# Kernel optimization log

Hardware: AMD Instinct MI355X
Metric: run time of the kernel (lower is better)

## Reference

```python
import jax, jax.numpy as jnp
import numpy as np

N = 150000          # active 4D voxels
K = 81              # 3^4 kernel offsets for 4D sparse conv, kernel_size=3
C_HID = 8           # MinkUNet14 INIT_DIM / stem+head planes
B, T, Z, Y, X = 2, 4, 32, 256, 256  # batch + output_grid [T,Z,Y,X]


def setup_inputs() -> dict:
    key = jax.random.key(0)
    k1, k2, k3, k4, k5, k6, k7, k8, k9 = jax.random.split(key, 9)
    feats = jnp.ones((N, 1), dtype=jnp.float32)  # module uses all-ones features
    # precomputed rulebook: neighbor index per kernel offset, with validity mask
    nbr_idx = jax.random.randint(k1, (N, K), 0, N, dtype=jnp.int32)
    nbr_mask = jax.random.randint(k2, (N, K), 0, 2, dtype=jnp.int32)
    # output voxel coordinates (x, y, z, t) and batch index, in-range
    cx = jax.random.randint(k3, (N,), 0, X, dtype=jnp.int32)
    cy = jax.random.randint(k4, (N,), 0, Y, dtype=jnp.int32)
    cz = jax.random.randint(k5, (N,), 0, Z, dtype=jnp.int32)
    ct = jax.random.randint(k6, (N,), 0, T, dtype=jnp.int32)
    coords = jnp.stack([cx, cy, cz, ct], axis=1)
    batch_idx = jax.random.randint(k7, (N,), 0, B, dtype=jnp.int32)
    # conv weights: [K, C_in, C_out]
    w1 = jax.random.normal(k8, (K, 1, C_HID), dtype=jnp.float32) * 0.1
    w2 = jax.random.normal(k9, (K, C_HID, C_HID), dtype=jnp.float32) * 0.05
    w_out = jax.random.normal(jax.random.fold_in(key, 99), (C_HID, 1), dtype=jnp.float32) * 0.1
    return {"feats": feats, "w1": w1, "w2": w2, "w_out": w_out,
            "nbr_idx": nbr_idx, "nbr_mask": nbr_mask,
            "coords": coords, "batch_idx": batch_idx}


def reference(feats, w1, w2, w_out, nbr_idx, nbr_mask, coords, batch_idx):
    mask = nbr_mask.astype(feats.dtype)[:, :, None]  # [N, K, 1]

    def sparse_conv(x, w):
        # gather-GEMM-scatter sparse conv: gather neighbors, implicit GEMM over offsets
        g = x[nbr_idx] * mask                 # [N, K, C_in]
        return jnp.einsum('nkc,kcd->nd', g, w)  # [N, C_out]

    h = jax.nn.relu(sparse_conv(feats, w1))   # 1 -> 8
    h = jax.nn.relu(sparse_conv(h, w2))       # 8 -> 8
    out_feats = h @ w_out                     # 8 -> 1 (out_channels=1)

    # dense scatter: dense_F[b, :, x, y, z, t] = feats, then permute(0,5,4,3,2,1)+squeeze
    # equivalent to scattering directly into [B, T, Z, Y, X]
    dense = jnp.zeros((B, T, Z, Y, X), dtype=feats.dtype)
    dense = dense.at[batch_idx, coords[:, 3], coords[:, 2], coords[:, 1], coords[:, 0]].set(out_feats[:, 0])
    return dense
```

## Files before the change

kernel.cpp:

```cpp
#include <hip/hip_runtime.h>
#include <hip/hip_fp16.h>


#define KK 81
#define CH 8
#define NS 21
#define TT 4
#define ZZ 32
#define YY 256
#define XX 256

typedef __attribute__((ext_vector_type(8))) _Float16 half8;
typedef __attribute__((ext_vector_type(4))) float f32x4;

__global__ __launch_bounds__(256) void k_h1b(const float* __restrict__ w1,
                                             const float* __restrict__ w2,
                                             const int* __restrict__ nbr_mask,
                                             half8* __restrict__ h1,
                                             uint4* __restrict__ bits4,
                                             half8* __restrict__ Btab, int n_total) {
    __shared__ int lm[256 * 27];
    const int tid = threadIdx.x;
    const int n0 = blockIdx.x * 256;
    const int n = n0 + tid;

    if (blockIdx.x < NS && tid < 64) {
        int s = blockIdx.x, q = tid >> 4, d = tid & 15;
        int kk = 4 * s + q;
        half8 b;
#pragma unroll
        for (int j = 0; j < CH; j++)
            b[j] = (d < CH && kk < KK) ? (_Float16)w2[(kk * CH + j) * CH + d]
                                       : (_Float16)0.f;
        Btab[s * 64 + tid] = b;
    }
    if (blockIdx.x == 0 && tid == 0) {
        half8 z;
#pragma unroll
        for (int c = 0; c < CH; c++) z[c] = (_Float16)0.f;
        h1[n_total] = z;
    }

    float acc[CH] = {0.f, 0.f, 0.f, 0.f, 0.f, 0.f, 0.f, 0.f};
    unsigned cb[3];
#pragma unroll
    for (int ch = 0; ch < 3; ch++) {
#pragma unroll
        for (int j = 0; j < 27; j++) {
            int i = tid + j * 256;
            int r = i / 27, c = i - r * 27;
            int srcn = n0 + r; if (srcn >= n_total) srcn = n_total - 1;
            lm[i] = nbr_mask[(long)srcn * KK + ch * 27 + c];
        }
        __syncthreads();
        unsigned cbits = 0;
        const int* row = lm + tid * 27;
#pragma unroll
        for (int kk = 0; kk < 27; kk++) {
            int m = row[kk];
            cbits |= (unsigned)(m & 1) << kk;
            float fm = (float)m;
            const float* wp = w1 + (ch * 27 + kk) * CH;
#pragma unroll
            for (int c = 0; c < CH; c++) acc[c] += fm * wp[c];
        }
        cb[ch] = cbits;
        __syncthreads();
    }

    if (n < n_total) {
        half8 r;
#pragma unroll
        for (int c = 0; c < CH; c++) r[c] = (_Float16)fmaxf(acc[c], 0.f);
        h1[n] = r;
        uint4 bw;
        bw.x = cb[0] | (cb[1] << 27);
        bw.y = (cb[1] >> 5) | (cb[2] << 22);
        bw.z = cb[2] >> 10;
        bw.w = 0u;
        bits4[n] = bw;
    }
}

__global__ __launch_bounds__(256, 4) void k_h2m(const half8* __restrict__ h1,
                                                const half8* __restrict__ Btab,
                                                const int* __restrict__ nbr_idx,
                                                const uint4* __restrict__ bits4,
                                                const float* __restrict__ w_out,
                                                float* __restrict__ outf,
                                                int n_total) {
    __shared__ int4 sB[NS * 64];
    __shared__ int  sidx[4 * 1300];
    const int tid = threadIdx.x;
    const int lane = tid & 63, wid = tid >> 6;
    const int m = lane & 15, q = lane >> 4;

    const int rw = blockIdx.x * 64 + (wid << 4);
    int wb = rw;
    if (wb + 16 > n_total) wb = n_total - 16;

    {
        int4* dst = (int4*)(sidx + wid * 1300);
        const int4* gsrc = (const int4*)(nbr_idx + (size_t)wb * KK);
#pragma unroll
        for (int j = 0; j < 6; j++) {
            int li = lane + j * 64;
            if (li < 324) dst[li] = gsrc[li];
        }
    }
    {
        const int4* gB = (const int4*)Btab;
#pragma unroll
        for (int j = 0; j < 6; j++) {
            int i = tid + j * 256;
            if (i < NS * 64) sB[i] = gB[i];
        }
    }
    __syncthreads();

    const int rowc = wb + m;
    const uint4 bw = bits4[rowc];
    const int* mi = sidx + wid * 1300 + m * KK + q;

    f32x4 acc0 = {0.f, 0.f, 0.f, 0.f};
    f32x4 acc1 = {0.f, 0.f, 0.f, 0.f};
#pragma unroll
    for (int s = 0; s < NS; s++) {
        const unsigned word = (s < 8) ? bw.x : (s < 16) ? bw.y : bw.z;
        const unsigned bit = (word >> ((4 * s + q) & 31)) & 1u;
        const unsigned ixr = (unsigned)mi[4 * s];
        const unsigned ix = bit ? ixr : (unsigned)n_total;
        half8 a = h1[ix];
        half8 b = *(const half8*)&sB[s * 64 + lane];
        if (s & 1) acc1 = __builtin_amdgcn_mfma_f32_16x16x32_f16(a, b, acc1, 0, 0, 0);
        else       acc0 = __builtin_amdgcn_mfma_f32_16x16x32_f16(a, b, acc0, 0, 0, 0);
    }
    f32x4 acc = acc0 + acc1;

    float wo = (m < CH) ? w_out[m] : 0.f;
    float v0 = fmaxf(acc[0], 0.f) * wo, v1 = fmaxf(acc[1], 0.f) * wo;
    float v2 = fmaxf(acc[2], 0.f) * wo, v3 = fmaxf(acc[3], 0.f) * wo;
#pragma unroll
    for (int off = 1; off < 16; off <<= 1) {
        v0 += __shfl_xor(v0, off, 16);
        v1 += __shfl_xor(v1, off, 16);
        v2 += __shfl_xor(v2, off, 16);
        v3 += __shfl_xor(v3, off, 16);
    }
    if (m == 0) {
        int gn = rw + q * 4;
        if (gn + 0 < n_total) outf[gn + 0] = v0;
        if (gn + 1 < n_total) outf[gn + 1] = v1;
        if (gn + 2 < n_total) outf[gn + 2] = v2;
        if (gn + 3 < n_total) outf[gn + 3] = v3;
    }
}

__device__ __forceinline__ int cell_of(const int* coords, const int* batch, int n) {
    int4 c = *(const int4*)(coords + 4 * n);
    int b = batch[n];
    return (((b * TT + c.w) * ZZ + c.z) * YY + c.y) * XX + c.x;
}

__global__ __launch_bounds__(256) void k_scat_max(const int* __restrict__ coords,
                                                  const int* __restrict__ batch,
                                                  int* __restrict__ dsti, int n_total) {
    int n = blockIdx.x * blockDim.x + threadIdx.x;
    if (n >= n_total) return;
    atomicMax(dsti + cell_of(coords, batch, n), n + 1);
}

__global__ __launch_bounds__(256) void k_scat_write(const int* __restrict__ coords,
                                                    const int* __restrict__ batch,
                                                    const float* __restrict__ outf,
                                                    int* dsti, float* dstf, int n_total) {
    int n = blockIdx.x * blockDim.x + threadIdx.x;
    if (n >= n_total) return;
    int cell = cell_of(coords, batch, n);
    if (dsti[cell] == n + 1) dstf[cell] = outf[n];
}

extern "C" void kernel_launch(void* const* d_in, const int* in_sizes, int n_in,
                              void* d_out, int out_size, void* d_ws, size_t ws_size,
                              hipStream_t stream) {
    const float* w1       = (const float*)d_in[1];
    const float* w2       = (const float*)d_in[2];
    const float* w_out    = (const float*)d_in[3];
    const int*   nbr_idx  = (const int*)d_in[4];
    const int*   nbr_mask = (const int*)d_in[5];
    const int*   coords   = (const int*)d_in[6];
    const int*   batch    = (const int*)d_in[7];

    int n_total = in_sizes[0];

    half8* h1    = (half8*)d_ws;
    uint4* bits4 = (uint4*)((char*)d_ws + (size_t)(n_total + 1) * sizeof(half8));
    float* outf  = (float*)((char*)bits4 + (size_t)n_total * sizeof(uint4));
    half8* Btab  = (half8*)(outf + n_total);
    float* out   = (float*)d_out;

    hipMemsetAsync(out, 0, (size_t)out_size * sizeof(float), stream);

    int nb = (n_total + 255) / 256;
    k_h1b<<<nb, 256, 0, stream>>>(w1, w2, nbr_mask, h1, bits4, Btab, n_total);
    int nb2 = (n_total + 63) / 64;
    k_h2m<<<nb2, 256, 0, stream>>>(h1, Btab, nbr_idx, bits4, w_out, outf, n_total);
    k_scat_max<<<nb, 256, 0, stream>>>(coords, batch, (int*)out, n_total);
    k_scat_write<<<nb, 256, 0, stream>>>(coords, batch, outf, (int*)out, out, n_total);
}
```

Baseline: 210.0 us.

## Fuse scatter atomicMax and final write into conv kernels, skip masked gathers

Moves the last-writer atomicMax pass into the first conv kernel and the conditional dense write into the MFMA kernel's epilogue. This removes two kernel launches and the intermediate outf buffer round trip. It also replaces the redirect-to-zero-row gather with a predicated load, so masked neighbors issue no memory access. The trade-off is that atomics now compete with h1 work, and the epilogue adds scalar loads of coords and the winner index on a single lane per row group.

```diff
diff --git a/kernel.cpp b/kernel.cpp
--- a/kernel.cpp
+++ b/kernel.cpp
@@ -13,16 +13,27 @@
 typedef __attribute__((ext_vector_type(8))) _Float16 half8;
 typedef __attribute__((ext_vector_type(4))) float f32x4;
 
+__device__ __forceinline__ int cell_of(const int* coords, const int* batch, int n) {
+    int4 c = *(const int4*)(coords + 4 * n);
+    int b = batch[n];
+    return (((b * TT + c.w) * ZZ + c.z) * YY + c.y) * XX + c.x;
+}
+
 __global__ __launch_bounds__(256) void k_h1b(const float* __restrict__ w1,
                                              const float* __restrict__ w2,
                                              const int* __restrict__ nbr_mask,
+                                             const int* __restrict__ coords,
+                                             const int* __restrict__ batch,
                                              half8* __restrict__ h1,
                                              uint4* __restrict__ bits4,
-                                             half8* __restrict__ Btab, int n_total) {
+                                             half8* __restrict__ Btab,
+                                             int* __restrict__ dsti, int n_total) {
     __shared__ int lm[256 * 27];
     const int tid = threadIdx.x;
     const int n0 = blockIdx.x * 256;
     const int n = n0 + tid;
+
+    if (n < n_total) atomicMax(dsti + cell_of(coords, batch, n), n + 1);
 
     if (blockIdx.x < NS && tid < 64) {
         int s = blockIdx.x, q = tid >> 4, d = tid & 15;
@@ -87,7 +98,9 @@
                                                 const int* __restrict__ nbr_idx,
                                                 const uint4* __restrict__ bits4,
                                                 const float* __restrict__ w_out,
-                                                float* __restrict__ outf,
+                                                const int* __restrict__ coords,
+                                                const int* __restrict__ batch,
+                                                float* __restrict__ dstf,
                                                 int n_total) {
     __shared__ int4 sB[NS * 64];
     __shared__ int  sidx[4 * 1300];
@@ -129,8 +142,9 @@
         const unsigned word = (s < 8) ? bw.x : (s < 16) ? bw.y : bw.z;
         const unsigned bit = (word >> ((4 * s + q) & 31)) & 1u;
         const unsigned ixr = (unsigned)mi[4 * s];
-        const unsigned ix = bit ? ixr : (unsigned)n_total;
-        half8 a = h1[ix];
+        half8 a = {(_Float16)0.f, (_Float16)0.f, (_Float16)0.f, (_Float16)0.f,
+                   (_Float16)0.f, (_Float16)0.f, (_Float16)0.f, (_Float16)0.f};
+        if (bit) a = h1[ixr];
         half8 b = *(const half8*)&sB[s * 64 + lane];
         if (s & 1) acc1 = __builtin_amdgcn_mfma_f32_16x16x32_f16(a, b, acc1, 0, 0, 0);
         else       acc0 = __builtin_amdgcn_mfma_f32_16x16x32_f16(a, b, acc0, 0, 0, 0);
@@ -148,36 +162,17 @@
         v3 += __shfl_xor(v3, off, 16);
     }
     if (m == 0) {
+        const int* dsti = (const int*)dstf;
         int gn = rw + q * 4;
-        if (gn + 0 < n_total) outf[gn + 0] = v0;
-        if (gn + 1 < n_total) outf[gn + 1] = v1;
-        if (gn + 2 < n_total) outf[gn + 2] = v2;
-        if (gn + 3 < n_total) outf[gn + 3] = v3;
-    }
-}
-
-__device__ __forceinline__ int cell_of(const int* coords, const int* batch, int n) {
-    int4 c = *(const int4*)(coords + 4 * n);
-    int b = batch[n];
-    return (((b * TT + c.w) * ZZ + c.z) * YY + c.y) * XX + c.x;
-}
-
-__global__ __launch_bounds__(256) void k_scat_max(const int* __restrict__ coords,
-                                                  const int* __restrict__ batch,
-                                                  int* __restrict__ dsti, int n_total) {
-    int n = blockIdx.x * blockDim.x + threadIdx.x;
-    if (n >= n_total) return;
-    atomicMax(dsti + cell_of(coords, batch, n), n + 1);
-}
-
-__global__ __launch_bounds__(256) void k_scat_write(const int* __restrict__ coords,
-                                                    const int* __restrict__ batch,
-                                                    const float* __restrict__ outf,
-                                                    int* dsti, float* dstf, int n_total) {
-    int n = blockIdx.x * blockDim.x + threadIdx.x;
-    if (n >= n_total) return;
-    int cell = cell_of(coords, batch, n);
-    if (dsti[cell] == n + 1) dstf[cell] = outf[n];
+        if (gn + 0 < n_total) { int c0 = cell_of(coords, batch, gn + 0);
+                                if (dsti[c0] == gn + 1) dstf[c0] = v0; }
+        if (gn + 1 < n_total) { int c1 = cell_of(coords, batch, gn + 1);
+                                if (dsti[c1] == gn + 2) dstf[c1] = v1; }
+        if (gn + 2 < n_total) { int c2 = cell_of(coords, batch, gn + 2);
+                                if (dsti[c2] == gn + 3) dstf[c2] = v2; }
+        if (gn + 3 < n_total) { int c3 = cell_of(coords, batch, gn + 3);
+                                if (dsti[c3] == gn + 4) dstf[c3] = v3; }
+    }
 }
 
 extern "C" void kernel_launch(void* const* d_in, const int* in_sizes, int n_in,
@@ -195,16 +190,15 @@
 
     half8* h1    = (half8*)d_ws;
     uint4* bits4 = (uint4*)((char*)d_ws + (size_t)(n_total + 1) * sizeof(half8));
-    float* outf  = (float*)((char*)bits4 + (size_t)n_total * sizeof(uint4));
-    half8* Btab  = (half8*)(outf + n_total);
+    half8* Btab  = (half8*)((char*)bits4 + (size_t)n_total * sizeof(uint4));
     float* out   = (float*)d_out;
 
     hipMemsetAsync(out, 0, (size_t)out_size * sizeof(float), stream);
 
     int nb = (n_total + 255) / 256;
-    k_h1b<<<nb, 256, 0, stream>>>(w1, w2, nbr_mask, h1, bits4, Btab, n_total);
+    k_h1b<<<nb, 256, 0, stream>>>(w1, w2, nbr_mask, coords, batch,
+                                  h1, bits4, Btab, (int*)out, n_total);
     int nb2 = (n_total + 63) / 64;
-    k_h2m<<<nb2, 256, 0, stream>>>(h1, Btab, nbr_idx, bits4, w_out, outf, n_total);
-    k_scat_max<<<nb, 256, 0, stream>>>(coords, batch, (int*)out, n_total);
-    k_scat_write<<<nb, 256, 0, stream>>>(coords, batch, outf, (int*)out, out, n_total);
-}
+    k_h2m<<<nb2, 256, 0, stream>>>(h1, Btab, nbr_idx, bits4, w_out,
+                                   coords, batch, out, n_total);
+}
```

After: 221.4 us. +5.4%, slower.
